# Performance work log

Hardware: AMD Instinct MI355X
Metric: run time of the kernel (lower is better)

The kernel has to match this reference:

```python
import jax, jax.numpy as jnp
import numpy as np

BS, S, H = 32, 2048, 1024

def setup_inputs() -> dict:
    key = jax.random.key(0)
    k1, k2, k3, k4 = jax.random.split(key, 4)
    hidden = jax.random.normal(k1, (BS, H), dtype=jnp.float32)
    encoder_outputs = jax.random.normal(k2, (BS, S, H), dtype=jnp.float32)
    # nn.Linear(H, H): weight [H, H], bias [H], kaiming-uniform-ish init
    bound = 1.0 / np.sqrt(H)
    W = jax.random.uniform(k3, (H, H), dtype=jnp.float32, minval=-bound, maxval=bound)
    b = jax.random.uniform(k4, (H,), dtype=jnp.float32, minval=-bound, maxval=bound)
    return {"hidden": hidden, "encoder_outputs": encoder_outputs, "W": W, "b": b}

def reference(hidden, encoder_outputs, W, b):
    # energy_i = Linear(enc_i); score_i = sum(hidden * energy_i); softmax over seq
    energy = jnp.einsum('bsh,kh->bsk', encoder_outputs, W) + b  # [BS, S, H]
    scores = jnp.einsum('bsh,bh->bs', energy, hidden)           # [BS, S]
    return jax.nn.softmax(scores, axis=-1)
```

## Files before the change

### kernel.cpp

```cpp
#include <hip/hip_runtime.h>
#include <math.h>

#define BS 32
#define S  2048
#define H  1024

__global__ __launch_bounds__(256) void compute_v(const float* __restrict__ hidden,
                                                 const float* __restrict__ W,
                                                 float* __restrict__ v) {
    __shared__ float hid[H];
    const int b   = blockIdx.y;
    const int tid = threadIdx.x;

    const float4* hid4 = (const float4*)(hidden + b * H);
    ((float4*)hid)[tid] = hid4[tid];
    __syncthreads();

    const int h = blockIdx.x * 256 + tid;
    float acc = 0.f;
#pragma unroll 8
    for (int k = 0; k < H; ++k) {
        acc = fmaf(W[k * H + h], hid[k], acc);
    }
    v[b * H + h] = acc;
}

__global__ __launch_bounds__(256) void compute_scores(const float* __restrict__ enc,
                                                      const float* __restrict__ v,
                                                      float* __restrict__ scores) {
    const int b    = blockIdx.y;
    const int tid  = threadIdx.x;
    const int wave = tid >> 6;
    const int lane = tid & 63;

    const float4* v4 = (const float4*)(v + b * H);
    float4 vr[4];
#pragma unroll
    for (int it = 0; it < 4; ++it) vr[it] = v4[it * 64 + lane];

    const int s0 = blockIdx.x * 64 + wave * 16;
    const float4* encb = (const float4*)enc + (size_t)b * S * (H / 4);

#pragma unroll 2
    for (int i = 0; i < 16; ++i) {
        const int s = s0 + i;
        const float4* e4 = encb + (size_t)s * (H / 4);
        float acc = 0.f;
#pragma unroll
        for (int it = 0; it < 4; ++it) {
            float4 e = e4[it * 64 + lane];
            acc = fmaf(e.x, vr[it].x, acc);
            acc = fmaf(e.y, vr[it].y, acc);
            acc = fmaf(e.z, vr[it].z, acc);
            acc = fmaf(e.w, vr[it].w, acc);
        }
#pragma unroll
        for (int off = 32; off > 0; off >>= 1)
            acc += __shfl_down(acc, off, 64);
        if (lane == 0) scores[b * S + s] = acc;
    }
}

__global__ __launch_bounds__(256) void softmax_rows(float* __restrict__ scores) {
    const int b    = blockIdx.x;
    const int tid  = threadIdx.x;
    const int wave = tid >> 6;
    const int lane = tid & 63;
    __shared__ float red[4];

    float x[8];
    float m = -INFINITY;
#pragma unroll
    for (int i = 0; i < 8; ++i) {
        x[i] = scores[b * S + tid + i * 256];
        m = fmaxf(m, x[i]);
    }
#pragma unroll
    for (int off = 1; off < 64; off <<= 1)
        m = fmaxf(m, __shfl_xor(m, off, 64));
    if (lane == 0) red[wave] = m;
    __syncthreads();
    m = fmaxf(fmaxf(red[0], red[1]), fmaxf(red[2], red[3]));

    float sum = 0.f;
#pragma unroll
    for (int i = 0; i < 8; ++i) {
        x[i] = __expf(x[i] - m);
        sum += x[i];
    }
#pragma unroll
    for (int off = 1; off < 64; off <<= 1)
        sum += __shfl_xor(sum, off, 64);
    __syncthreads();
    if (lane == 0) red[wave] = sum;
    __syncthreads();
    sum = (red[0] + red[1]) + (red[2] + red[3]);
    const float inv = 1.0f / sum;

#pragma unroll
    for (int i = 0; i < 8; ++i)
        scores[b * S + tid + i * 256] = x[i] * inv;
}

extern "C" void kernel_launch(void* const* d_in, const int* in_sizes, int n_in,
                              void* d_out, int out_size, void* d_ws, size_t ws_size,
                              hipStream_t stream) {
    const float* hidden = (const float*)d_in[0];
    const float* enc    = (const float*)d_in[1];
    const float* W      = (const float*)d_in[2];

    float* v      = (float*)d_ws;
    float* outp   = (float*)d_out;

    dim3 g1(H / 256, BS);
    compute_v<<<g1, 256, 0, stream>>>(hidden, W, v);

    dim3 g2(S / 64, BS);
    compute_scores<<<g2, 256, 0, stream>>>(enc, v, outp);

    softmax_rows<<<BS, 256, 0, stream>>>(outp);
}
```

Measured before the change: 431.6 us.

## Split-K the hidden projection and batch four rows per score reduction

compute_v now splits the 1024-long reduction across the four waves of a block, each covering 256 k values. The partial sums are combined through shared memory. The grid grows from 128 to 512 blocks, so the W-times-hidden matvec has more parallelism and a shorter serial dependency chain. compute_scores now handles four sequence rows per step with independent accumulators, reads enc with nontemporal loads, and reduces all four rows together with xor shuffles. This adds memory-level parallelism to the streaming pass, at the risk of higher register use and a dynamically indexed accumulator array when lanes 0-3 store their results.

New measurement: 358.7 us. -16.9%, faster.

```diff
diff --git a/kernel.cpp b/kernel.cpp
--- a/kernel.cpp
+++ b/kernel.cpp
@@ -5,24 +5,35 @@
 #define S  2048
 #define H  1024
 
+typedef float vfloat4 __attribute__((ext_vector_type(4)));
+
 __global__ __launch_bounds__(256) void compute_v(const float* __restrict__ hidden,
                                                  const float* __restrict__ W,
                                                  float* __restrict__ v) {
     __shared__ float hid[H];
-    const int b   = blockIdx.y;
-    const int tid = threadIdx.x;
+    __shared__ float part[4][64];
+    const int b    = blockIdx.y;
+    const int tid  = threadIdx.x;
+    const int wave = tid >> 6;
+    const int lane = tid & 63;
 
-    const float4* hid4 = (const float4*)(hidden + b * H);
-    ((float4*)hid)[tid] = hid4[tid];
+    ((float4*)hid)[tid] = ((const float4*)(hidden + b * H))[tid];
     __syncthreads();
 
-    const int h = blockIdx.x * 256 + tid;
+    const int h = blockIdx.x * 64 + lane;
+    const float* Wp = W + (size_t)(wave * 256) * H + h;
+    const float* hp = hid + wave * 256;
     float acc = 0.f;
 #pragma unroll 8
-    for (int k = 0; k < H; ++k) {
-        acc = fmaf(W[k * H + h], hid[k], acc);
+    for (int k = 0; k < 256; ++k)
+        acc = fmaf(Wp[(size_t)k * H], hp[k], acc);
+
+    part[wave][lane] = acc;
+    __syncthreads();
+    if (wave == 0) {
+        float r = (part[0][lane] + part[1][lane]) + (part[2][lane] + part[3][lane]);
+        v[b * H + h] = r;
     }
-    v[b * H + h] = acc;
 }
 
 __global__ __launch_bounds__(256) void compute_scores(const float* __restrict__ enc,
@@ -39,25 +50,31 @@
     for (int it = 0; it < 4; ++it) vr[it] = v4[it * 64 + lane];
 
     const int s0 = blockIdx.x * 64 + wave * 16;
-    const float4* encb = (const float4*)enc + (size_t)b * S * (H / 4);
+    const vfloat4* encb = (const vfloat4*)enc + (size_t)b * S * (H / 4);
 
-#pragma unroll 2
-    for (int i = 0; i < 16; ++i) {
-        const int s = s0 + i;
-        const float4* e4 = encb + (size_t)s * (H / 4);
-        float acc = 0.f;
 #pragma unroll
-        for (int it = 0; it < 4; ++it) {
-            float4 e = e4[it * 64 + lane];
-            acc = fmaf(e.x, vr[it].x, acc);
-            acc = fmaf(e.y, vr[it].y, acc);
-            acc = fmaf(e.z, vr[it].z, acc);
-            acc = fmaf(e.w, vr[it].w, acc);
+    for (int i = 0; i < 16; i += 4) {
+        float acc[4] = {0.f, 0.f, 0.f, 0.f};
+#pragma unroll
+        for (int j = 0; j < 4; ++j) {
+            const vfloat4* e4 = encb + (size_t)(s0 + i + j) * (H / 4);
+#pragma unroll
+            for (int it = 0; it < 4; ++it) {
+                vfloat4 e = __builtin_nontemporal_load(&e4[it * 64 + lane]);
+                acc[j] = fmaf(e.x, vr[it].x, acc[j]);
+                acc[j] = fmaf(e.y, vr[it].y, acc[j]);
+                acc[j] = fmaf(e.z, vr[it].z, acc[j]);
+                acc[j] = fmaf(e.w, vr[it].w, acc[j]);
+            }
         }
 #pragma unroll
-        for (int off = 32; off > 0; off >>= 1)
-            acc += __shfl_down(acc, off, 64);
-        if (lane == 0) scores[b * S + s] = acc;
+        for (int off = 32; off > 0; off >>= 1) {
+#pragma unroll
+            for (int j = 0; j < 4; ++j)
+                acc[j] += __shfl_xor(acc[j], off, 64);
+        }
+        if (lane < 4)
+            scores[b * S + s0 + i + lane] = acc[lane];
     }
 }
 
@@ -109,10 +126,10 @@
     const float* enc    = (const float*)d_in[1];
     const float* W      = (const float*)d_in[2];
 
-    float* v      = (float*)d_ws;
-    float* outp   = (float*)d_out;
+    float* v    = (float*)d_ws;
+    float* outp = (float*)d_out;
 
-    dim3 g1(H / 256, BS);
+    dim3 g1(H / 64, BS);
     compute_v<<<g1, 256, 0, stream>>>(hidden, W, v);
 
     dim3 g2(S / 64, BS);
```
